# Kernel optimization log

Measured on AMD Instinct MI355X. Metric: run time of the kernel, lower is better.

## Reference

```python
import jax, jax.numpy as jnp
import numpy as np

E = 256   # hidden_dim
H = 2     # num_heads
DH = E // H
EPS = 1e-5


def setup_inputs() -> dict:
    key = jax.random.key(0)
    ks = jax.random.split(key, 20)
    L, S, MAXLOOP = 8192, 8192, 16
    rel = jax.random.randint(ks[0], (L, MAXLOOP), 0, S)
    # sprinkle some padding sentinels (-1 / -2) like real edge loops
    pad = jax.random.uniform(ks[1], (L, MAXLOOP)) < 0.25
    rel = jnp.where(pad, -1, rel)
    rel = rel.at[:, 0].set(jnp.abs(rel[:, 0]) % S)  # ensure >=1 valid edge per face
    inp = {
        'v_face_edge_loop': rel.astype(jnp.int64) if jax.config.jax_enable_x64 else rel.astype(jnp.int32),
        'v_face_mask': jnp.ones((L,), dtype=bool),
        'v_edge_embedding': jax.random.normal(ks[2], (S, E), jnp.float32),
        'v_face_embedding': jax.random.normal(ks[3], (L, E), jnp.float32),
    }
    def w(k, shape):
        return (jax.random.normal(k, shape, jnp.float32) * 0.02)
    for i, base in ((1, 4), (2, 10)):
        inp[f'w_in{i}'] = w(ks[base + 0], (3 * E, E))
        inp[f'b_in{i}'] = jnp.zeros((3 * E,), jnp.float32)
        inp[f'w_out{i}'] = w(ks[base + 1], (E, E))
        inp[f'b_out{i}'] = jnp.zeros((E,), jnp.float32)
        inp[f'ln{i}_g'] = jnp.ones((E,), jnp.float32)
        inp[f'ln{i}_b'] = jnp.zeros((E,), jnp.float32)
    return inp


def _build_mask(face_edge_loop, S):
    # True = disallowed (torch bool attn_mask semantics).
    L = face_edge_loop.shape[0]
    rel = face_edge_loop
    invalid = (rel == -1) | (rel == -2)
    rel = jnp.where(invalid, S, rel)  # scatter invalids into sentinel column S
    mask = jnp.ones((L, S + 1), dtype=bool)
    mask = mask.at[jnp.arange(L)[:, None], rel].set(False)
    return mask[:, :S]  # [L, S]


def _mha(x, kv, mask, w_in, b_in, w_out, b_out):
    # torch nn.MultiheadAttention (unbatched, eval/no-dropout)
    wq, wk, wv = jnp.split(w_in, 3, axis=0)
    bq, bk, bv = jnp.split(b_in, 3, axis=0)
    L, S = x.shape[0], kv.shape[0]
    q = (x @ wq.T + bq).reshape(L, H, DH)
    k = (kv @ wk.T + bk).reshape(S, H, DH)
    v = (kv @ wv.T + bv).reshape(S, H, DH)
    scores = jnp.einsum('lhd,shd->hls', q, k) / np.sqrt(DH).astype(np.float32)
    scores = jnp.where(mask[None, :, :], jnp.float32(-1e9), scores)
    attn = jax.nn.softmax(scores, axis=-1)          # [H, L, S]
    out = jnp.einsum('hls,shd->lhd', attn, v).reshape(L, E)
    return out @ w_out.T + b_out


def _layernorm(x, g, b):
    m = x.mean(-1, keepdims=True)
    var = ((x - m) ** 2).mean(-1, keepdims=True)
    return (x - m) / jnp.sqrt(var + EPS) * g + b


def reference(v_face_edge_loop, v_face_mask, v_edge_embedding, v_face_embedding,
              w_in1, b_in1, w_out1, b_out1, ln1_g, ln1_b,
              w_in2, b_in2, w_out2, b_out2, ln2_g, ln2_b):
    S = v_edge_embedding.shape[0]
    # v_face_mask is all-True here (static shapes); loop[mask] == loop
    mask = _build_mask(v_face_edge_loop, S)
    x = v_face_embedding
    x = x + _mha(x, v_edge_embedding, mask, w_in1, b_in1, w_out1, b_out1)
    x = _layernorm(x, ln1_g, ln1_b)
    x = x + _mha(x, v_edge_embedding, mask, w_in2, b_in2, w_out2, b_out2)
    x = _layernorm(x, ln2_g, ln2_b)
    return x
```

## Files before the change

### kernel.cpp

```cpp
#include <hip/hip_runtime.h>
#include <hip/hip_bf16.h>

typedef short short8 __attribute__((ext_vector_type(8)));
typedef short short4v __attribute__((ext_vector_type(4)));
typedef float f32x4 __attribute__((ext_vector_type(4)));

#define E 256
#define DH 128

__device__ __forceinline__ float bf2f(__hip_bfloat16 x) { return __bfloat162float(x); }
__device__ __forceinline__ __hip_bfloat16 f2bf(float x) { return __float2bfloat16(x); }

struct CvtArgs { const float* in[6]; __hip_bfloat16* out[6]; int n[6]; };

__global__ __launch_bounds__(256) void f2b_all(CvtArgs a)
{
    int seg = blockIdx.y;
    int i = (blockIdx.x * 256 + threadIdx.x) * 8;
    if (i >= a.n[seg]) return;
    const float* in = a.in[seg];
    float4 x = *reinterpret_cast<const float4*>(in + i);
    float4 y = *reinterpret_cast<const float4*>(in + i + 4);
    __hip_bfloat16* o = a.out[seg] + i;
    o[0] = f2bf(x.x); o[1] = f2bf(x.y); o[2] = f2bf(x.z); o[3] = f2bf(x.w);
    o[4] = f2bf(y.x); o[5] = f2bf(y.y); o[6] = f2bf(y.z); o[7] = f2bf(y.w);
}

struct ProjSeg { const __hip_bfloat16* A; const __hip_bfloat16* W; const float* b; __hip_bfloat16* out; };
struct ProjArgs { ProjSeg seg[5]; };

__global__ __launch_bounds__(256) void gemm_proj(ProjArgs args, int M)
{
    int wv = threadIdx.x >> 6, lane = threadIdx.x & 63;
    int m0 = blockIdx.x * 32;
    if (m0 >= M) return;
    ProjSeg sg = args.seg[blockIdx.y];
    int lo = lane & 15, hi = lane >> 4;

    const __hip_bfloat16* arow0 = sg.A + (size_t)(m0 + lo) * E + hi * 8;
    const __hip_bfloat16* arow1 = arow0 + 16 * E;
    const __hip_bfloat16* brow  = sg.W + (size_t)(wv * 64 + lo) * E + hi * 8;

    f32x4 acc[2][4] = {};
#pragma unroll
    for (int k = 0; k < 8; ++k) {
        short8 a0 = *reinterpret_cast<const short8*>(arow0 + k * 32);
        short8 a1 = *reinterpret_cast<const short8*>(arow1 + k * 32);
#pragma unroll
        for (int nt = 0; nt < 4; ++nt) {
            short8 b = *reinterpret_cast<const short8*>(brow + (size_t)nt * 16 * E + k * 32);
            acc[0][nt] = __builtin_amdgcn_mfma_f32_16x16x32_bf16(a0, b, acc[0][nt], 0, 0, 0);
            acc[1][nt] = __builtin_amdgcn_mfma_f32_16x16x32_bf16(a1, b, acc[1][nt], 0, 0, 0);
        }
    }
#pragma unroll
    for (int nt = 0; nt < 4; ++nt) {
        int col = wv * 64 + nt * 16 + lo;
        float bias = sg.b[col];
#pragma unroll
        for (int mt = 0; mt < 2; ++mt)
#pragma unroll
            for (int r = 0; r < 4; ++r) {
                int row = m0 + mt * 16 + hi * 4 + r;
                sg.out[(size_t)row * E + col] = f2bf(acc[mt][nt][r] + bias);
            }
    }
}

__global__ __launch_bounds__(1024) void attn_outproj_ln(
    const int* __restrict__ rel, const __hip_bfloat16* __restrict__ q16,
    const __hip_bfloat16* __restrict__ k16, const __hip_bfloat16* __restrict__ v16,
    const __hip_bfloat16* __restrict__ wout, const float* __restrict__ bout,
    const float* __restrict__ resid, const float* __restrict__ lng, const float* __restrict__ lnb,
    float* __restrict__ xres_out, __hip_bfloat16* __restrict__ xbf_out,
    float* __restrict__ final_out, int L, int ML)
{
    __shared__ __align__(16) __hip_bfloat16 atile[16 * 264];
    __shared__ __align__(16) float sm[16 * 260];
    __shared__ __align__(16) float lds_w[16][2][16];
    __shared__ int lds_idx[16][16];

    int tid = threadIdx.x, wv = tid >> 6, lane = tid & 63;
    int m0 = blockIdx.x * 16;
    int g = lane >> 2, q = lane & 3;
    int face = m0 + wv;
    const float scale = 0.088388347648318447f;

    const int* rr = rel + (size_t)face * ML;
    int myidx = (g < ML) ? rr[g] : -1;

    bool dup = false;
#pragma unroll
    for (int d = 1; d < 16; ++d) {
        int other = __shfl(myidx, ((g - d) & 15) * 4 + q);
        if (d <= g && other == myidx) dup = true;
    }
    bool myuse = (myidx >= 0) && !dup;
    int safe = myidx < 0 ? 0 : myidx;
    if (q == 0) lds_idx[wv][g] = safe;

#pragma unroll
    for (int h = 0; h < 2; ++h) {
        const __hip_bfloat16* kbase = k16 + (size_t)safe * E + h * DH;
        const __hip_bfloat16* qbase = q16 + (size_t)face * E + h * DH;
        float part = 0.f;
#pragma unroll
        for (int t = 0; t < 4; ++t) {
            short8 qv = *reinterpret_cast<const short8*>(qbase + (t * 4 + q) * 8);
            short8 kv = *reinterpret_cast<const short8*>(kbase + (t * 4 + q) * 8);
            const __hip_bfloat16* qp = (const __hip_bfloat16*)&qv;
            const __hip_bfloat16* kp = (const __hip_bfloat16*)&kv;
#pragma unroll
            for (int e2 = 0; e2 < 8; ++e2)
                part += bf2f(qp[e2]) * bf2f(kp[e2]);
        }
        part += __shfl_xor(part, 1);
        part += __shfl_xor(part, 2);
        float sc = myuse ? part * scale : -1e30f;
        float mx = sc;
#pragma unroll
        for (int off = 4; off < 64; off <<= 1) mx = fmaxf(mx, __shfl_xor(mx, off));
        float e = __expf(sc - mx);
        float den = e;
#pragma unroll
        for (int off = 4; off < 64; off <<= 1) den += __shfl_xor(den, off);
        if (q == 0) lds_w[wv][h][g] = e / den;
    }

    {
        int h = lane >> 5;
        float a0 = 0.f, a1 = 0.f, a2 = 0.f, a3 = 0.f;
#pragma unroll
        for (int j = 0; j < 16; ++j) {
            int ij = lds_idx[wv][j];
            float wj = lds_w[wv][h][j];
            short4v vv = *reinterpret_cast<const short4v*>(v16 + (size_t)ij * E + 4 * lane);
            const __hip_bfloat16* vp = (const __hip_bfloat16*)&vv;
            a0 += wj * bf2f(vp[0]);
            a1 += wj * bf2f(vp[1]);
            a2 += wj * bf2f(vp[2]);
            a3 += wj * bf2f(vp[3]);
        }
        __hip_bfloat16 ob[4] = {f2bf(a0), f2bf(a1), f2bf(a2), f2bf(a3)};
        *reinterpret_cast<short4v*>(atile + wv * 264 + 4 * lane) =
            *reinterpret_cast<const short4v*>(ob);
    }
    __syncthreads();

    {
        int lo = lane & 15, hi = lane >> 4;
        const __hip_bfloat16* arow = atile + lo * 264 + hi * 8;
        const __hip_bfloat16* brow = wout + (size_t)(wv * 16 + lo) * E + hi * 8;
        f32x4 acc = {0.f, 0.f, 0.f, 0.f};
#pragma unroll
        for (int kk = 0; kk < 8; ++kk) {
            short8 a = *reinterpret_cast<const short8*>(arow + kk * 32);
            short8 b = *reinterpret_cast<const short8*>(brow + kk * 32);
            acc = __builtin_amdgcn_mfma_f32_16x16x32_bf16(a, b, acc, 0, 0, 0);
        }
        int col = wv * 16 + lo;
#pragma unroll
        for (int r = 0; r < 4; ++r)
            sm[(hi * 4 + r) * 260 + col] = acc[r];
    }
    __syncthreads();

    {
        int rowg = m0 + wv;
        float4 pv = *reinterpret_cast<const float4*>(sm + wv * 260 + 4 * lane);
        float4 rv = *reinterpret_cast<const float4*>(resid + (size_t)rowg * E + 4 * lane);
        float4 bb = *reinterpret_cast<const float4*>(bout + 4 * lane);
        float v0 = pv.x + bb.x + rv.x;
        float v1 = pv.y + bb.y + rv.y;
        float v2 = pv.z + bb.z + rv.z;
        float v3 = pv.w + bb.w + rv.w;
        float s  = v0 + v1 + v2 + v3;
        float s2 = v0 * v0 + v1 * v1 + v2 * v2 + v3 * v3;
#pragma unroll
        for (int off = 1; off < 64; off <<= 1) {
            s  += __shfl_xor(s, off);
            s2 += __shfl_xor(s2, off);
        }
        float mean = s * (1.f / 256.f);
        float var  = s2 * (1.f / 256.f) - mean * mean;
        float rstd = rsqrtf(var + 1e-5f);
        float4 gg = *reinterpret_cast<const float4*>(lng + 4 * lane);
        float4 b2 = *reinterpret_cast<const float4*>(lnb + 4 * lane);
        float y0 = (v0 - mean) * rstd * gg.x + b2.x;
        float y1 = (v1 - mean) * rstd * gg.y + b2.y;
        float y2 = (v2 - mean) * rstd * gg.z + b2.z;
        float y3 = (v3 - mean) * rstd * gg.w + b2.w;
        if (final_out) {
            float4 o = {y0, y1, y2, y3};
            *reinterpret_cast<float4*>(final_out + (size_t)rowg * E + 4 * lane) = o;
        } else {
            float4 o = {y0, y1, y2, y3};
            *reinterpret_cast<float4*>(xres_out + (size_t)rowg * E + 4 * lane) = o;
            __hip_bfloat16 ob[4] = {f2bf(y0), f2bf(y1), f2bf(y2), f2bf(y3)};
            *reinterpret_cast<short4v*>(xbf_out + (size_t)rowg * E + 4 * lane) =
                *reinterpret_cast<const short4v*>(ob);
        }
    }
}

extern "C" void kernel_launch(void* const* d_in, const int* in_sizes, int n_in,
                              void* d_out, int out_size, void* d_ws, size_t ws_size,
                              hipStream_t stream) {
    const int* rel = (const int*)d_in[0];
    const float* edge = (const float*)d_in[2];
    const float* face = (const float*)d_in[3];
    const float* w_in[2]  = {(const float*)d_in[4],  (const float*)d_in[10]};
    const float* b_in[2]  = {(const float*)d_in[5],  (const float*)d_in[11]};
    const float* w_out[2] = {(const float*)d_in[6],  (const float*)d_in[12]};
    const float* b_out[2] = {(const float*)d_in[7],  (const float*)d_in[13]};
    const float* ln_g[2]  = {(const float*)d_in[8],  (const float*)d_in[14]};
    const float* ln_b[2]  = {(const float*)d_in[9],  (const float*)d_in[15]};

    int S = in_sizes[2] / E;
    int L = in_sizes[3] / E;
    int ML = in_sizes[0] / L;

    char* ws = (char*)d_ws;
    __hip_bfloat16* face16 = (__hip_bfloat16*)ws; ws += (size_t)L * E * 2;
    __hip_bfloat16* edge16 = (__hip_bfloat16*)ws; ws += (size_t)S * E * 2;
    __hip_bfloat16* q16    = (__hip_bfloat16*)ws; ws += (size_t)L * E * 2;
    __hip_bfloat16* k16[2], *v16[2];
    for (int l = 0; l < 2; ++l) {
        k16[l] = (__hip_bfloat16*)ws; ws += (size_t)S * E * 2;
        v16[l] = (__hip_bfloat16*)ws; ws += (size_t)S * E * 2;
    }
    __hip_bfloat16* xbf = (__hip_bfloat16*)ws;    ws += (size_t)L * E * 2;
    float* xres = (float*)ws;                     ws += (size_t)L * E * 4;
    __hip_bfloat16* win16[2], *wout16[2];
    for (int l = 0; l < 2; ++l) {
        win16[l]  = (__hip_bfloat16*)ws; ws += (size_t)3 * E * E * 2;
        wout16[l] = (__hip_bfloat16*)ws; ws += (size_t)E * E * 2;
    }

    float* outp = (float*)d_out;

    {
        CvtArgs ca;
        ca.in[0] = face;     ca.out[0] = face16;    ca.n[0] = L * E;
        ca.in[1] = edge;     ca.out[1] = edge16;    ca.n[1] = S * E;
        ca.in[2] = w_in[0];  ca.out[2] = win16[0];  ca.n[2] = 3 * E * E;
        ca.in[3] = w_in[1];  ca.out[3] = win16[1];  ca.n[3] = 3 * E * E;
        ca.in[4] = w_out[0]; ca.out[4] = wout16[0]; ca.n[4] = E * E;
        ca.in[5] = w_out[1]; ca.out[5] = wout16[1]; ca.n[5] = E * E;
        int gx = (L * E) / (256 * 8);
        f2b_all<<<dim3(gx, 6), 256, 0, stream>>>(ca);
    }

    {
        ProjArgs pa;
        pa.seg[0] = {face16, win16[0],                     b_in[0],         q16};
        pa.seg[1] = {edge16, win16[0] + (size_t)E * E,     b_in[0] + E,     k16[0]};
        pa.seg[2] = {edge16, win16[0] + (size_t)2 * E * E, b_in[0] + 2 * E, v16[0]};
        pa.seg[3] = {edge16, win16[1] + (size_t)E * E,     b_in[1] + E,     k16[1]};
        pa.seg[4] = {edge16, win16[1] + (size_t)2 * E * E, b_in[1] + 2 * E, v16[1]};
        gemm_proj<<<dim3(L / 32, 5), 256, 0, stream>>>(pa, L);
    }

    attn_outproj_ln<<<L / 16, 1024, 0, stream>>>(rel, q16, k16[0], v16[0],
                                                 wout16[0], b_out[0], face,
                                                 ln_g[0], ln_b[0],
                                                 xres, xbf, nullptr, L, ML);

    {
        ProjArgs pa;
        pa.seg[0] = {xbf, win16[1], b_in[1], q16};
        gemm_proj<<<dim3(L / 32, 1), 256, 0, stream>>>(pa, L);
    }

    attn_outproj_ln<<<L / 16, 1024, 0, stream>>>(rel, q16, k16[1], v16[1],
                                                 wout16[1], b_out[1], xres,
                                                 ln_g[1], ln_b[1],
                                                 nullptr, nullptr, outp, L, ML);
}
```

Baseline: 182.8 us.

## Fuse fp32-to-bf16 conversion into projection GEMM and restructure attention block

The projection GEMM now reads fp32 activations directly for the face and residual inputs and converts them in registers. This removes the separate face16 and xbf conversion buffers and their global round-trips. The attention kernel moves from 1024 to 512 threads, with each wave handling two faces and two output-column tiles. LayerNorm is done from MFMA registers through a cross-wave LDS reduction instead of an LDS staging tile. Vectorized bf16 stores replace scalar stores in the convert kernel, at the cost of more fp32 load bandwidth in the GEMM.

```diff
diff --git a/kernel.cpp b/kernel.cpp
--- a/kernel.cpp
+++ b/kernel.cpp
@@ -11,7 +11,13 @@
 __device__ __forceinline__ float bf2f(__hip_bfloat16 x) { return __bfloat162float(x); }
 __device__ __forceinline__ __hip_bfloat16 f2bf(float x) { return __float2bfloat16(x); }
 
-struct CvtArgs { const float* in[6]; __hip_bfloat16* out[6]; int n[6]; };
+__device__ __forceinline__ short8 cvt8(float4 a, float4 b) {
+    __hip_bfloat16 t[8] = {f2bf(a.x), f2bf(a.y), f2bf(a.z), f2bf(a.w),
+                           f2bf(b.x), f2bf(b.y), f2bf(b.z), f2bf(b.w)};
+    return *reinterpret_cast<const short8*>(t);
+}
+
+struct CvtArgs { const float* in[5]; __hip_bfloat16* out[5]; int n[5]; };
 
 __global__ __launch_bounds__(256) void f2b_all(CvtArgs a)
 {
@@ -21,12 +27,11 @@
     const float* in = a.in[seg];
     float4 x = *reinterpret_cast<const float4*>(in + i);
     float4 y = *reinterpret_cast<const float4*>(in + i + 4);
-    __hip_bfloat16* o = a.out[seg] + i;
-    o[0] = f2bf(x.x); o[1] = f2bf(x.y); o[2] = f2bf(x.z); o[3] = f2bf(x.w);
-    o[4] = f2bf(y.x); o[5] = f2bf(y.y); o[6] = f2bf(y.z); o[7] = f2bf(y.w);
-}
-
-struct ProjSeg { const __hip_bfloat16* A; const __hip_bfloat16* W; const float* b; __hip_bfloat16* out; };
+    *reinterpret_cast<short8*>(a.out[seg] + i) = cvt8(x, y);
+}
+
+struct ProjSeg { const float* Af; const __hip_bfloat16* Ab;
+                 const __hip_bfloat16* W; const float* b; __hip_bfloat16* out; };
 struct ProjArgs { ProjSeg seg[5]; };
 
 __global__ __launch_bounds__(256) void gemm_proj(ProjArgs args, int M)
@@ -37,20 +42,38 @@
     ProjSeg sg = args.seg[blockIdx.y];
     int lo = lane & 15, hi = lane >> 4;
 
-    const __hip_bfloat16* arow0 = sg.A + (size_t)(m0 + lo) * E + hi * 8;
-    const __hip_bfloat16* arow1 = arow0 + 16 * E;
-    const __hip_bfloat16* brow  = sg.W + (size_t)(wv * 64 + lo) * E + hi * 8;
+    const __hip_bfloat16* brow = sg.W + (size_t)(wv * 64 + lo) * E + hi * 8;
 
     f32x4 acc[2][4] = {};
-#pragma unroll
-    for (int k = 0; k < 8; ++k) {
-        short8 a0 = *reinterpret_cast<const short8*>(arow0 + k * 32);
-        short8 a1 = *reinterpret_cast<const short8*>(arow1 + k * 32);
-#pragma unroll
-        for (int nt = 0; nt < 4; ++nt) {
-            short8 b = *reinterpret_cast<const short8*>(brow + (size_t)nt * 16 * E + k * 32);
-            acc[0][nt] = __builtin_amdgcn_mfma_f32_16x16x32_bf16(a0, b, acc[0][nt], 0, 0, 0);
-            acc[1][nt] = __builtin_amdgcn_mfma_f32_16x16x32_bf16(a1, b, acc[1][nt], 0, 0, 0);
+    if (sg.Af) {
+        const float* ar0 = sg.Af + (size_t)(m0 + lo) * E + hi * 8;
+        const float* ar1 = ar0 + 16 * E;
+#pragma unroll
+        for (int k = 0; k < 8; ++k) {
+            short8 a0 = cvt8(*reinterpret_cast<const float4*>(ar0 + k * 32),
+                             *reinterpret_cast<const float4*>(ar0 + k * 32 + 4));
+            short8 a1 = cvt8(*reinterpret_cast<const float4*>(ar1 + k * 32),
+                             *reinterpret_cast<const float4*>(ar1 + k * 32 + 4));
+#pragma unroll
+            for (int nt = 0; nt < 4; ++nt) {
+                short8 b = *reinterpret_cast<const short8*>(brow + (size_t)nt * 16 * E + k * 32);
+                acc[0][nt] = __builtin_amdgcn_mfma_f32_16x16x32_bf16(a0, b, acc[0][nt], 0, 0, 0);
+                acc[1][nt] = __builtin_amdgcn_mfma_f32_16x16x32_bf16(a1, b, acc[1][nt], 0, 0, 0);
+            }
+        }
+    } else {
+        const __hip_bfloat16* ar0 = sg.Ab + (size_t)(m0 + lo) * E + hi * 8;
+        const __hip_bfloat16* ar1 = ar0 + 16 * E;
+#pragma unroll
+        for (int k = 0; k < 8; ++k) {
+            short8 a0 = *reinterpret_cast<const short8*>(ar0 + k * 32);
+            short8 a1 = *reinterpret_cast<const short8*>(ar1 + k * 32);
+#pragma unroll
+            for (int nt = 0; nt < 4; ++nt) {
+                short8 b = *reinterpret_cast<const short8*>(brow + (size_t)nt * 16 * E + k * 32);
+                acc[0][nt] = __builtin_amdgcn_mfma_f32_16x16x32_bf16(a0, b, acc[0][nt], 0, 0, 0);
+                acc[1][nt] = __builtin_amdgcn_mfma_f32_16x16x32_bf16(a1, b, acc[1][nt], 0, 0, 0);
+            }
         }
     }
 #pragma unroll
@@ -67,90 +90,97 @@
     }
 }
 
-__global__ __launch_bounds__(1024) void attn_outproj_ln(
+__global__ __launch_bounds__(512, 4) void attn_outproj_ln(
     const int* __restrict__ rel, const __hip_bfloat16* __restrict__ q16,
     const __hip_bfloat16* __restrict__ k16, const __hip_bfloat16* __restrict__ v16,
     const __hip_bfloat16* __restrict__ wout, const float* __restrict__ bout,
     const float* __restrict__ resid, const float* __restrict__ lng, const float* __restrict__ lnb,
-    float* __restrict__ xres_out, __hip_bfloat16* __restrict__ xbf_out,
-    float* __restrict__ final_out, int L, int ML)
+    float* __restrict__ outp, int L, int ML)
 {
     __shared__ __align__(16) __hip_bfloat16 atile[16 * 264];
-    __shared__ __align__(16) float sm[16 * 260];
     __shared__ __align__(16) float lds_w[16][2][16];
     __shared__ int lds_idx[16][16];
+    __shared__ float lds_s[16][8], lds_s2[16][8];
+    __shared__ float lds_mv[16], lds_rs[16];
 
     int tid = threadIdx.x, wv = tid >> 6, lane = tid & 63;
     int m0 = blockIdx.x * 16;
     int g = lane >> 2, q = lane & 3;
-    int face = m0 + wv;
     const float scale = 0.088388347648318447f;
 
-    const int* rr = rel + (size_t)face * ML;
-    int myidx = (g < ML) ? rr[g] : -1;
-
-    bool dup = false;
-#pragma unroll
-    for (int d = 1; d < 16; ++d) {
-        int other = __shfl(myidx, ((g - d) & 15) * 4 + q);
-        if (d <= g && other == myidx) dup = true;
-    }
-    bool myuse = (myidx >= 0) && !dup;
-    int safe = myidx < 0 ? 0 : myidx;
-    if (q == 0) lds_idx[wv][g] = safe;
-
-#pragma unroll
-    for (int h = 0; h < 2; ++h) {
-        const __hip_bfloat16* kbase = k16 + (size_t)safe * E + h * DH;
-        const __hip_bfloat16* qbase = q16 + (size_t)face * E + h * DH;
-        float part = 0.f;
-#pragma unroll
-        for (int t = 0; t < 4; ++t) {
-            short8 qv = *reinterpret_cast<const short8*>(qbase + (t * 4 + q) * 8);
-            short8 kv = *reinterpret_cast<const short8*>(kbase + (t * 4 + q) * 8);
-            const __hip_bfloat16* qp = (const __hip_bfloat16*)&qv;
-            const __hip_bfloat16* kp = (const __hip_bfloat16*)&kv;
-#pragma unroll
-            for (int e2 = 0; e2 < 8; ++e2)
-                part += bf2f(qp[e2]) * bf2f(kp[e2]);
-        }
-        part += __shfl_xor(part, 1);
-        part += __shfl_xor(part, 2);
-        float sc = myuse ? part * scale : -1e30f;
-        float mx = sc;
-#pragma unroll
-        for (int off = 4; off < 64; off <<= 1) mx = fmaxf(mx, __shfl_xor(mx, off));
-        float e = __expf(sc - mx);
-        float den = e;
-#pragma unroll
-        for (int off = 4; off < 64; off <<= 1) den += __shfl_xor(den, off);
-        if (q == 0) lds_w[wv][h][g] = e / den;
-    }
-
-    {
-        int h = lane >> 5;
-        float a0 = 0.f, a1 = 0.f, a2 = 0.f, a3 = 0.f;
-#pragma unroll
-        for (int j = 0; j < 16; ++j) {
-            int ij = lds_idx[wv][j];
-            float wj = lds_w[wv][h][j];
-            short4v vv = *reinterpret_cast<const short4v*>(v16 + (size_t)ij * E + 4 * lane);
-            const __hip_bfloat16* vp = (const __hip_bfloat16*)&vv;
-            a0 += wj * bf2f(vp[0]);
-            a1 += wj * bf2f(vp[1]);
-            a2 += wj * bf2f(vp[2]);
-            a3 += wj * bf2f(vp[3]);
-        }
-        __hip_bfloat16 ob[4] = {f2bf(a0), f2bf(a1), f2bf(a2), f2bf(a3)};
-        *reinterpret_cast<short4v*>(atile + wv * 264 + 4 * lane) =
-            *reinterpret_cast<const short4v*>(ob);
+#pragma unroll
+    for (int it = 0; it < 2; ++it) {
+        int r = wv * 2 + it;
+        int face = m0 + r;
+        const int* rr = rel + (size_t)face * ML;
+        int myidx = (g < ML) ? rr[g] : -1;
+
+        bool dup = false;
+#pragma unroll
+        for (int d = 1; d < 16; ++d) {
+            int other = __shfl(myidx, ((g - d) & 15) * 4 + q);
+            if (d <= g && other == myidx) dup = true;
+        }
+        bool myuse = (myidx >= 0) && !dup;
+        int safe = myidx < 0 ? 0 : myidx;
+        if (q == 0) lds_idx[r][g] = safe;
+
+#pragma unroll
+        for (int h = 0; h < 2; ++h) {
+            const __hip_bfloat16* kbase = k16 + (size_t)safe * E + h * DH;
+            const __hip_bfloat16* qbase = q16 + (size_t)face * E + h * DH;
+            float part = 0.f;
+#pragma unroll
+            for (int t = 0; t < 4; ++t) {
+                short8 qv = *reinterpret_cast<const short8*>(qbase + (t * 4 + q) * 8);
+                short8 kv = *reinterpret_cast<const short8*>(kbase + (t * 4 + q) * 8);
+                const __hip_bfloat16* qp = (const __hip_bfloat16*)&qv;
+                const __hip_bfloat16* kp = (const __hip_bfloat16*)&kv;
+#pragma unroll
+                for (int e2 = 0; e2 < 8; ++e2)
+                    part += bf2f(qp[e2]) * bf2f(kp[e2]);
+            }
+            part += __shfl_xor(part, 1);
+            part += __shfl_xor(part, 2);
+            float sc = myuse ? part * scale : -1e30f;
+            float mx = sc;
+#pragma unroll
+            for (int off = 4; off < 64; off <<= 1) mx = fmaxf(mx, __shfl_xor(mx, off));
+            float e = __expf(sc - mx);
+            float den = e;
+#pragma unroll
+            for (int off = 4; off < 64; off <<= 1) den += __shfl_xor(den, off);
+            if (q == 0) lds_w[r][h][g] = e / den;
+        }
+
+        {
+            int h = lane >> 5;
+            float a0 = 0.f, a1 = 0.f, a2 = 0.f, a3 = 0.f;
+#pragma unroll
+            for (int j = 0; j < 16; ++j) {
+                int ij = lds_idx[r][j];
+                float wj = lds_w[r][h][j];
+                short4v vv = *reinterpret_cast<const short4v*>(v16 + (size_t)ij * E + 4 * lane);
+                const __hip_bfloat16* vp = (const __hip_bfloat16*)&vv;
+                a0 += wj * bf2f(vp[0]);
+                a1 += wj * bf2f(vp[1]);
+                a2 += wj * bf2f(vp[2]);
+                a3 += wj * bf2f(vp[3]);
+            }
+            __hip_bfloat16 ob[4] = {f2bf(a0), f2bf(a1), f2bf(a2), f2bf(a3)};
+            *reinterpret_cast<short4v*>(atile + r * 264 + 4 * lane) =
+                *reinterpret_cast<const short4v*>(ob);
+        }
     }
     __syncthreads();
 
-    {
-        int lo = lane & 15, hi = lane >> 4;
+    int lo = lane & 15, hi = lane >> 4;
+    float val[2][4];
+#pragma unroll
+    for (int nt = 0; nt < 2; ++nt) {
+        int n0 = wv * 32 + nt * 16;
         const __hip_bfloat16* arow = atile + lo * 264 + hi * 8;
-        const __hip_bfloat16* brow = wout + (size_t)(wv * 16 + lo) * E + hi * 8;
+        const __hip_bfloat16* brow = wout + (size_t)(n0 + lo) * E + hi * 8;
         f32x4 acc = {0.f, 0.f, 0.f, 0.f};
 #pragma unroll
         for (int kk = 0; kk < 8; ++kk) {
@@ -158,47 +188,54 @@
             short8 b = *reinterpret_cast<const short8*>(brow + kk * 32);
             acc = __builtin_amdgcn_mfma_f32_16x16x32_bf16(a, b, acc, 0, 0, 0);
         }
-        int col = wv * 16 + lo;
-#pragma unroll
-        for (int r = 0; r < 4; ++r)
-            sm[(hi * 4 + r) * 260 + col] = acc[r];
+        float bias = bout[n0 + lo];
+#pragma unroll
+        for (int r2 = 0; r2 < 4; ++r2) {
+            int rowg = m0 + hi * 4 + r2;
+            val[nt][r2] = acc[r2] + bias + resid[(size_t)rowg * E + n0 + lo];
+        }
+    }
+    float s[4], s2[4];
+#pragma unroll
+    for (int r2 = 0; r2 < 4; ++r2) {
+        s[r2]  = val[0][r2] + val[1][r2];
+        s2[r2] = val[0][r2] * val[0][r2] + val[1][r2] * val[1][r2];
+    }
+#pragma unroll
+    for (int off = 1; off < 16; off <<= 1) {
+#pragma unroll
+        for (int r2 = 0; r2 < 4; ++r2) {
+            s[r2]  += __shfl_xor(s[r2], off);
+            s2[r2] += __shfl_xor(s2[r2], off);
+        }
+    }
+    if (lo == 0) {
+#pragma unroll
+        for (int r2 = 0; r2 < 4; ++r2) {
+            lds_s[hi * 4 + r2][wv]  = s[r2];
+            lds_s2[hi * 4 + r2][wv] = s2[r2];
+        }
     }
     __syncthreads();
-
-    {
-        int rowg = m0 + wv;
-        float4 pv = *reinterpret_cast<const float4*>(sm + wv * 260 + 4 * lane);
-        float4 rv = *reinterpret_cast<const float4*>(resid + (size_t)rowg * E + 4 * lane);
-        float4 bb = *reinterpret_cast<const float4*>(bout + 4 * lane);
-        float v0 = pv.x + bb.x + rv.x;
-        float v1 = pv.y + bb.y + rv.y;
-        float v2 = pv.z + bb.z + rv.z;
-        float v3 = pv.w + bb.w + rv.w;
-        float s  = v0 + v1 + v2 + v3;
-        float s2 = v0 * v0 + v1 * v1 + v2 * v2 + v3 * v3;
-#pragma unroll
-        for (int off = 1; off < 64; off <<= 1) {
-            s  += __shfl_xor(s, off);
-            s2 += __shfl_xor(s2, off);
-        }
-        float mean = s * (1.f / 256.f);
-        float var  = s2 * (1.f / 256.f) - mean * mean;
-        float rstd = rsqrtf(var + 1e-5f);
-        float4 gg = *reinterpret_cast<const float4*>(lng + 4 * lane);
-        float4 b2 = *reinterpret_cast<const float4*>(lnb + 4 * lane);
-        float y0 = (v0 - mean) * rstd * gg.x + b2.x;
-        float y1 = (v1 - mean) * rstd * gg.y + b2.y;
-        float y2 = (v2 - mean) * rstd * gg.z + b2.z;
-        float y3 = (v3 - mean) * rstd * gg.w + b2.w;
-        if (final_out) {
-            float4 o = {y0, y1, y2, y3};
-            *reinterpret_cast<float4*>(final_out + (size_t)rowg * E + 4 * lane) = o;
-        } else {
-            float4 o = {y0, y1, y2, y3};
-            *reinterpret_cast<float4*>(xres_out + (size_t)rowg * E + 4 * lane) = o;
-            __hip_bfloat16 ob[4] = {f2bf(y0), f2bf(y1), f2bf(y2), f2bf(y3)};
-            *reinterpret_cast<short4v*>(xbf_out + (size_t)rowg * E + 4 * lane) =
-                *reinterpret_cast<const short4v*>(ob);
+    if (wv == 0 && lane < 16) {
+        float S = 0.f, S2 = 0.f;
+#pragma unroll
+        for (int w = 0; w < 8; ++w) { S += lds_s[lane][w]; S2 += lds_s2[lane][w]; }
+        float mean = S * (1.f / 256.f);
+        float var  = S2 * (1.f / 256.f) - mean * mean;
+        lds_mv[lane] = mean;
+        lds_rs[lane] = rsqrtf(var + 1e-5f);
+    }
+    __syncthreads();
+#pragma unroll
+    for (int nt = 0; nt < 2; ++nt) {
+        int col = wv * 32 + nt * 16 + lo;
+        float gg = lng[col], bb = lnb[col];
+#pragma unroll
+        for (int r2 = 0; r2 < 4; ++r2) {
+            int row = hi * 4 + r2;
+            float y = (val[nt][r2] - lds_mv[row]) * lds_rs[row] * gg + bb;
+            outp[(size_t)(m0 + row) * E + col] = y;
         }
     }
 }
@@ -221,7 +258,6 @@
     int ML = in_sizes[0] / L;
 
     char* ws = (char*)d_ws;
-    __hip_bfloat16* face16 = (__hip_bfloat16*)ws; ws += (size_t)L * E * 2;
     __hip_bfloat16* edge16 = (__hip_bfloat16*)ws; ws += (size_t)S * E * 2;
     __hip_bfloat16* q16    = (__hip_bfloat16*)ws; ws += (size_t)L * E * 2;
     __hip_bfloat16* k16[2], *v16[2];
@@ -229,7 +265,6 @@
         k16[l] = (__hip_bfloat16*)ws; ws += (size_t)S * E * 2;
         v16[l] = (__hip_bfloat16*)ws; ws += (size_t)S * E * 2;
     }
-    __hip_bfloat16* xbf = (__hip_bfloat16*)ws;    ws += (size_t)L * E * 2;
     float* xres = (float*)ws;                     ws += (size_t)L * E * 4;
     __hip_bfloat16* win16[2], *wout16[2];
     for (int l = 0; l < 2; ++l) {
@@ -241,39 +276,36 @@
 
     {
         CvtArgs ca;
-        ca.in[0] = face;     ca.out[0] = face16;    ca.n[0] = L * E;
-        ca.in[1] = edge;     ca.out[1] = edge16;    ca.n[1] = S * E;
-        ca.in[2] = w_in[0];  ca.out[2] = win16[0];  ca.n[2] = 3 * E * E;
-        ca.in[3] = w_in[1];  ca.out[3] = win16[1];  ca.n[3] = 3 * E * E;
-        ca.in[4] = w_out[0]; ca.out[4] = wout16[0]; ca.n[4] = E * E;
-        ca.in[5] = w_out[1]; ca.out[5] = wout16[1]; ca.n[5] = E * E;
-        int gx = (L * E) / (256 * 8);
-        f2b_all<<<dim3(gx, 6), 256, 0, stream>>>(ca);
+        ca.in[0] = edge;     ca.out[0] = edge16;    ca.n[0] = S * E;
+        ca.in[1] = w_in[0];  ca.out[1] = win16[0];  ca.n[1] = 3 * E * E;
+        ca.in[2] = w_in[1];  ca.out[2] = win16[1];  ca.n[2] = 3 * E * E;
+        ca.in[3] = w_out[0]; ca.out[3] = wout16[0]; ca.n[3] = E * E;
+        ca.in[4] = w_out[1]; ca.out[4] = wout16[1]; ca.n[4] = E * E;
+        int gx = (S * E) / (256 * 8);
+        f2b_all<<<dim3(gx, 5), 256, 0, stream>>>(ca);
     }
 
     {
         ProjArgs pa;
-        pa.seg[0] = {face16, win16[0],                     b_in[0],         q16};
-        pa.seg[1] = {edge16, win16[0] + (size_t)E * E,     b_in[0] + E,     k16[0]};
-        pa.seg[2] = {edge16, win16[0] + (size_t)2 * E * E, b_in[0] + 2 * E, v16[0]};
-        pa.seg[3] = {edge16, win16[1] + (size_t)E * E,     b_in[1] + E,     k16[1]};
-        pa.seg[4] = {edge16, win16[1] + (size_t)2 * E * E, b_in[1] + 2 * E, v16[1]};
+        pa.seg[0] = {face, nullptr,    win16[0],                     b_in[0],         q16};
+        pa.seg[1] = {nullptr, edge16,  win16[0] + (size_t)E * E,     b_in[0] + E,     k16[0]};
+        pa.seg[2] = {nullptr, edge16,  win16[0] + (size_t)2 * E * E, b_in[0] + 2 * E, v16[0]};
+        pa.seg[3] = {nullptr, edge16,  win16[1] + (size_t)E * E,     b_in[1] + E,     k16[1]};
+        pa.seg[4] = {nullptr, edge16,  win16[1] + (size_t)2 * E * E, b_in[1] + 2 * E, v16[1]};
         gemm_proj<<<dim3(L / 32, 5), 256, 0, stream>>>(pa, L);
     }
 
-    attn_outproj_ln<<<L / 16, 1024, 0, stream>>>(rel, q16, k16[0], v16[0],
-                                                 wout16[0], b_out[0], face,
-                                                 ln_g[0], ln_b[0],
-                                                 xres, xbf, nullptr, L, ML);
+    attn_outproj_ln<<<L / 16, 512, 0, stream>>>(rel, q16, k16[0], v16[0],
+                                                wout16[0], b_out[0], face,
+                                                ln_g[0], ln_b[0], xres, L, ML);
 
     {
         ProjArgs pa;
-        pa.seg[0] = {xbf, win16[1], b_in[1], q16};
+        pa.seg[0] = {xres, nullptr, win16[1], b_in[1], q16};
         gemm_proj<<<dim3(L / 32, 1), 256, 0, stream>>>(pa, L);
     }
 
-    attn_outproj_ln<<<L / 16, 1024, 0, stream>>>(rel, q16, k16[1], v16[1],
-                                                 wout16[1], b_out[1], xres,
-                                                 ln_g[1], ln_b[1],
-                                                 nullptr, nullptr, outp, L, ML);
-}
+    attn_outproj_ln<<<L / 16, 512, 0, stream>>>(rel, q16, k16[1], v16[1],
+                                                wout16[1], b_out[1], xres,
+                                                ln_g[1], ln_b[1], outp, L, ML);
+}
```

New measurement: 190.3 us. +4.1%, slower.

## Drop fp32-to-bf16 pre-pass and fuse layer-2 Q projection into attention kernel

Applied to the files above, without the earlier changes.

The standalone conversion kernel is removed. The projection GEMM and the out-projection now load fp32 activations and weights and convert them to bf16 in registers just before each MFMA. The separate layer-2 Q-projection GEMM is folded into the tail of the first attention/out-proj/LayerNorm kernel, which reuses the LDS tile holding the normalized rows. This cuts two launches and the round trips through the bf16 staging buffers. In exchange, fp32 weights are re-read and re-converted in every block, which doubles the load bytes for weights and A rows in the GEMM inner loops.

```diff
diff --git a/kernel.cpp b/kernel.cpp
--- a/kernel.cpp
+++ b/kernel.cpp
@@ -11,22 +11,17 @@
 __device__ __forceinline__ float bf2f(__hip_bfloat16 x) { return __bfloat162float(x); }
 __device__ __forceinline__ __hip_bfloat16 f2bf(float x) { return __float2bfloat16(x); }
 
-struct CvtArgs { const float* in[6]; __hip_bfloat16* out[6]; int n[6]; };
-
-__global__ __launch_bounds__(256) void f2b_all(CvtArgs a)
-{
-    int seg = blockIdx.y;
-    int i = (blockIdx.x * 256 + threadIdx.x) * 8;
-    if (i >= a.n[seg]) return;
-    const float* in = a.in[seg];
-    float4 x = *reinterpret_cast<const float4*>(in + i);
-    float4 y = *reinterpret_cast<const float4*>(in + i + 4);
-    __hip_bfloat16* o = a.out[seg] + i;
-    o[0] = f2bf(x.x); o[1] = f2bf(x.y); o[2] = f2bf(x.z); o[3] = f2bf(x.w);
-    o[4] = f2bf(y.x); o[5] = f2bf(y.y); o[6] = f2bf(y.z); o[7] = f2bf(y.w);
-}
-
-struct ProjSeg { const __hip_bfloat16* A; const __hip_bfloat16* W; const float* b; __hip_bfloat16* out; };
+__device__ __forceinline__ short8 cvt8(float4 a, float4 b) {
+    __hip_bfloat16 t[8] = {f2bf(a.x), f2bf(a.y), f2bf(a.z), f2bf(a.w),
+                           f2bf(b.x), f2bf(b.y), f2bf(b.z), f2bf(b.w)};
+    return *reinterpret_cast<const short8*>(t);
+}
+__device__ __forceinline__ short8 ld_cvt8(const float* p) {
+    return cvt8(*reinterpret_cast<const float4*>(p),
+                *reinterpret_cast<const float4*>(p + 4));
+}
+
+struct ProjSeg { const float* A; const float* W; const float* b; __hip_bfloat16* out; };
 struct ProjArgs { ProjSeg seg[5]; };
 
 __global__ __launch_bounds__(256) void gemm_proj(ProjArgs args, int M)
@@ -37,18 +32,18 @@
     ProjSeg sg = args.seg[blockIdx.y];
     int lo = lane & 15, hi = lane >> 4;
 
-    const __hip_bfloat16* arow0 = sg.A + (size_t)(m0 + lo) * E + hi * 8;
-    const __hip_bfloat16* arow1 = arow0 + 16 * E;
-    const __hip_bfloat16* brow  = sg.W + (size_t)(wv * 64 + lo) * E + hi * 8;
+    const float* ar0  = sg.A + (size_t)(m0 + lo) * E + hi * 8;
+    const float* ar1  = ar0 + 16 * E;
+    const float* brow = sg.W + (size_t)(wv * 64 + lo) * E + hi * 8;
 
     f32x4 acc[2][4] = {};
 #pragma unroll
     for (int k = 0; k < 8; ++k) {
-        short8 a0 = *reinterpret_cast<const short8*>(arow0 + k * 32);
-        short8 a1 = *reinterpret_cast<const short8*>(arow1 + k * 32);
+        short8 a0 = ld_cvt8(ar0 + k * 32);
+        short8 a1 = ld_cvt8(ar1 + k * 32);
 #pragma unroll
         for (int nt = 0; nt < 4; ++nt) {
-            short8 b = *reinterpret_cast<const short8*>(brow + (size_t)nt * 16 * E + k * 32);
+            short8 b = ld_cvt8(brow + (size_t)nt * 16 * E + k * 32);
             acc[0][nt] = __builtin_amdgcn_mfma_f32_16x16x32_bf16(a0, b, acc[0][nt], 0, 0, 0);
             acc[1][nt] = __builtin_amdgcn_mfma_f32_16x16x32_bf16(a1, b, acc[1][nt], 0, 0, 0);
         }
@@ -70,10 +65,11 @@
 __global__ __launch_bounds__(1024) void attn_outproj_ln(
     const int* __restrict__ rel, const __hip_bfloat16* __restrict__ q16,
     const __hip_bfloat16* __restrict__ k16, const __hip_bfloat16* __restrict__ v16,
-    const __hip_bfloat16* __restrict__ wout, const float* __restrict__ bout,
+    const float* __restrict__ wout, const float* __restrict__ bout,
     const float* __restrict__ resid, const float* __restrict__ lng, const float* __restrict__ lnb,
-    float* __restrict__ xres_out, __hip_bfloat16* __restrict__ xbf_out,
-    float* __restrict__ final_out, int L, int ML)
+    float* __restrict__ outp,
+    const float* __restrict__ wq1, const float* __restrict__ bq1,
+    __hip_bfloat16* __restrict__ q1out, int L, int ML)
 {
     __shared__ __align__(16) __hip_bfloat16 atile[16 * 264];
     __shared__ __align__(16) float sm[16 * 260];
@@ -147,15 +143,15 @@
     }
     __syncthreads();
 
-    {
-        int lo = lane & 15, hi = lane >> 4;
+    int lo = lane & 15, hi = lane >> 4;
+    {
         const __hip_bfloat16* arow = atile + lo * 264 + hi * 8;
-        const __hip_bfloat16* brow = wout + (size_t)(wv * 16 + lo) * E + hi * 8;
+        const float* browf = wout + (size_t)(wv * 16 + lo) * E + hi * 8;
         f32x4 acc = {0.f, 0.f, 0.f, 0.f};
 #pragma unroll
         for (int kk = 0; kk < 8; ++kk) {
             short8 a = *reinterpret_cast<const short8*>(arow + kk * 32);
-            short8 b = *reinterpret_cast<const short8*>(brow + kk * 32);
+            short8 b = ld_cvt8(browf + kk * 32);
             acc = __builtin_amdgcn_mfma_f32_16x16x32_bf16(a, b, acc, 0, 0, 0);
         }
         int col = wv * 16 + lo;
@@ -190,16 +186,31 @@
         float y1 = (v1 - mean) * rstd * gg.y + b2.y;
         float y2 = (v2 - mean) * rstd * gg.z + b2.z;
         float y3 = (v3 - mean) * rstd * gg.w + b2.w;
-        if (final_out) {
-            float4 o = {y0, y1, y2, y3};
-            *reinterpret_cast<float4*>(final_out + (size_t)rowg * E + 4 * lane) = o;
-        } else {
-            float4 o = {y0, y1, y2, y3};
-            *reinterpret_cast<float4*>(xres_out + (size_t)rowg * E + 4 * lane) = o;
+        float4 o = {y0, y1, y2, y3};
+        *reinterpret_cast<float4*>(outp + (size_t)rowg * E + 4 * lane) = o;
+        if (wq1) {
             __hip_bfloat16 ob[4] = {f2bf(y0), f2bf(y1), f2bf(y2), f2bf(y3)};
-            *reinterpret_cast<short4v*>(xbf_out + (size_t)rowg * E + 4 * lane) =
+            *reinterpret_cast<short4v*>(atile + wv * 264 + 4 * lane) =
                 *reinterpret_cast<const short4v*>(ob);
         }
+    }
+
+    if (wq1) {
+        __syncthreads();
+        const __hip_bfloat16* arow = atile + lo * 264 + hi * 8;
+        const float* browf = wq1 + (size_t)(wv * 16 + lo) * E + hi * 8;
+        f32x4 acc = {0.f, 0.f, 0.f, 0.f};
+#pragma unroll
+        for (int kk = 0; kk < 8; ++kk) {
+            short8 a = *reinterpret_cast<const short8*>(arow + kk * 32);
+            short8 b = ld_cvt8(browf + kk * 32);
+            acc = __builtin_amdgcn_mfma_f32_16x16x32_bf16(a, b, acc, 0, 0, 0);
+        }
+        int col = wv * 16 + lo;
+        float bias = bq1[col];
+#pragma unroll
+        for (int r = 0; r < 4; ++r)
+            q1out[(size_t)(m0 + hi * 4 + r) * E + col] = f2bf(acc[r] + bias);
     }
 }
 
@@ -221,59 +232,33 @@
     int ML = in_sizes[0] / L;
 
     char* ws = (char*)d_ws;
-    __hip_bfloat16* face16 = (__hip_bfloat16*)ws; ws += (size_t)L * E * 2;
-    __hip_bfloat16* edge16 = (__hip_bfloat16*)ws; ws += (size_t)S * E * 2;
-    __hip_bfloat16* q16    = (__hip_bfloat16*)ws; ws += (size_t)L * E * 2;
+    __hip_bfloat16* q16 = (__hip_bfloat16*)ws;    ws += (size_t)L * E * 2;
     __hip_bfloat16* k16[2], *v16[2];
     for (int l = 0; l < 2; ++l) {
         k16[l] = (__hip_bfloat16*)ws; ws += (size_t)S * E * 2;
         v16[l] = (__hip_bfloat16*)ws; ws += (size_t)S * E * 2;
     }
-    __hip_bfloat16* xbf = (__hip_bfloat16*)ws;    ws += (size_t)L * E * 2;
     float* xres = (float*)ws;                     ws += (size_t)L * E * 4;
-    __hip_bfloat16* win16[2], *wout16[2];
-    for (int l = 0; l < 2; ++l) {
-        win16[l]  = (__hip_bfloat16*)ws; ws += (size_t)3 * E * E * 2;
-        wout16[l] = (__hip_bfloat16*)ws; ws += (size_t)E * E * 2;
-    }
 
     float* outp = (float*)d_out;
 
     {
-        CvtArgs ca;
-        ca.in[0] = face;     ca.out[0] = face16;    ca.n[0] = L * E;
-        ca.in[1] = edge;     ca.out[1] = edge16;    ca.n[1] = S * E;
-        ca.in[2] = w_in[0];  ca.out[2] = win16[0];  ca.n[2] = 3 * E * E;
-        ca.in[3] = w_in[1];  ca.out[3] = win16[1];  ca.n[3] = 3 * E * E;
-        ca.in[4] = w_out[0]; ca.out[4] = wout16[0]; ca.n[4] = E * E;
-        ca.in[5] = w_out[1]; ca.out[5] = wout16[1]; ca.n[5] = E * E;
-        int gx = (L * E) / (256 * 8);
-        f2b_all<<<dim3(gx, 6), 256, 0, stream>>>(ca);
-    }
-
-    {
         ProjArgs pa;
-        pa.seg[0] = {face16, win16[0],                     b_in[0],         q16};
-        pa.seg[1] = {edge16, win16[0] + (size_t)E * E,     b_in[0] + E,     k16[0]};
-        pa.seg[2] = {edge16, win16[0] + (size_t)2 * E * E, b_in[0] + 2 * E, v16[0]};
-        pa.seg[3] = {edge16, win16[1] + (size_t)E * E,     b_in[1] + E,     k16[1]};
-        pa.seg[4] = {edge16, win16[1] + (size_t)2 * E * E, b_in[1] + 2 * E, v16[1]};
+        pa.seg[0] = {face, w_in[0],                     b_in[0],         q16};
+        pa.seg[1] = {edge, w_in[0] + (size_t)E * E,     b_in[0] + E,     k16[0]};
+        pa.seg[2] = {edge, w_in[0] + (size_t)2 * E * E, b_in[0] + 2 * E, v16[0]};
+        pa.seg[3] = {edge, w_in[1] + (size_t)E * E,     b_in[1] + E,     k16[1]};
+        pa.seg[4] = {edge, w_in[1] + (size_t)2 * E * E, b_in[1] + 2 * E, v16[1]};
         gemm_proj<<<dim3(L / 32, 5), 256, 0, stream>>>(pa, L);
     }
 
     attn_outproj_ln<<<L / 16, 1024, 0, stream>>>(rel, q16, k16[0], v16[0],
-                                                 wout16[0], b_out[0], face,
-                                                 ln_g[0], ln_b[0],
-                                                 xres, xbf, nullptr, L, ML);
-
-    {
-        ProjArgs pa;
-        pa.seg[0] = {xbf, win16[1], b_in[1], q16};
-        gemm_proj<<<dim3(L / 32, 1), 256, 0, stream>>>(pa, L);
-    }
+                                                 w_out[0], b_out[0], face,
+                                                 ln_g[0], ln_b[0], xres,
+                                                 w_in[1], b_in[1], q16, L, ML);
 
     attn_outproj_ln<<<L / 16, 1024, 0, stream>>>(rel, q16, k16[1], v16[1],
-                                                 wout16[1], b_out[1], xres,
-                                                 ln_g[1], ln_b[1],
-                                                 nullptr, nullptr, outp, L, ML);
-}
+                                                 w_out[1], b_out[1], xres,
+                                                 ln_g[1], ln_b[1], outp,
+                                                 nullptr, nullptr, nullptr, L, ML);
+}
```

Measured after the change: 224.1 us. 1.23x slower.
